# Kernel tuning notes

Measured on AMD Instinct MI355X. Metric: run time of the kernel, lower is better.

Reference implementation:

```python
import jax, jax.numpy as jnp
import numpy as np

D_MODEL = 1024
NUM_HEADS = 16
DEPTH = D_MODEL // NUM_HEADS


def setup_inputs() -> dict:
    key = jax.random.key(0)
    ks = jax.random.split(key, 5)
    s = 1.0 / np.sqrt(D_MODEL)
    return {
        "x": jax.random.normal(ks[0], (4, 2048, D_MODEL), dtype=jnp.float32),
        "wq": jax.random.normal(ks[1], (D_MODEL, D_MODEL), dtype=jnp.float32) * s,
        "bq": jnp.zeros((D_MODEL,), dtype=jnp.float32),
        "wk": jax.random.normal(ks[2], (D_MODEL, D_MODEL), dtype=jnp.float32) * s,
        "bk": jnp.zeros((D_MODEL,), dtype=jnp.float32),
        "wv": jax.random.normal(ks[3], (D_MODEL, D_MODEL), dtype=jnp.float32) * s,
        "bv": jnp.zeros((D_MODEL,), dtype=jnp.float32),
        "wo": jax.random.normal(ks[4], (D_MODEL, D_MODEL), dtype=jnp.float32) * s,
        "bo": jnp.zeros((D_MODEL,), dtype=jnp.float32),
    }


def reference(x, wq, bq, wk, bk, wv, bv, wo, bo):
    B, S, _ = x.shape
    def split_heads(t):  # [B,S,D] -> [B,H,S,depth]
        return t.reshape(B, S, NUM_HEADS, DEPTH).transpose(0, 2, 1, 3)
    q = split_heads(x @ wq + bq)
    k = split_heads(x @ wk + bk)
    v = split_heads(x @ wv + bv)
    scale = 1.0 / jnp.sqrt(jnp.float32(DEPTH))
    logits = jnp.einsum("bhqd,bhkd->bhqk", q, k) * scale
    attn = jax.nn.softmax(logits, axis=-1)  # dropout is identity at inference
    out = jnp.einsum("bhqk,bhkd->bhqd", attn, v)
    out = out.transpose(0, 2, 1, 3).reshape(B, S, D_MODEL)
    return out @ wo + bo
```

## Files before the change

### kernel.cpp

```cpp
#include <hip/hip_runtime.h>
#include <hip/hip_bf16.h>
#include <cstdint>
#include <cstddef>

typedef __attribute__((ext_vector_type(8))) short s8v;
typedef __attribute__((ext_vector_type(4))) float f4v;

#define MFMA_BF16(a, b, c) __builtin_amdgcn_mfma_f32_16x16x32_bf16((a), (b), (c), 0, 0, 0)

__device__ __forceinline__ short f2bf(float f) {
    unsigned u = __builtin_bit_cast(unsigned, f);
    u += 0x7FFFu + ((u >> 16) & 1u);
    return (short)(u >> 16);
}

__device__ __forceinline__ unsigned cvt_pk_bf16(float a, float b) {
    unsigned r;
    asm("v_cvt_pk_bf16_f32 %0, %1, %2" : "=v"(r) : "v"(a), "v"(b));
    return r;
}

#define GLDS16(gsrc, ldst)                                                                   \
    __builtin_amdgcn_global_load_lds(                                                        \
        (const __attribute__((address_space(1))) unsigned int*)(gsrc),                       \
        (__attribute__((address_space(3))) unsigned int*)(ldst), 16, 0, 0)

__global__ void convert_x(const float4* __restrict__ in, short4* __restrict__ out, int n4) {
    int i = blockIdx.x * blockDim.x + threadIdx.x;
    int stride = gridDim.x * blockDim.x;
    for (; i < n4; i += stride) {
        float4 v = in[i];
        short4 o;
        o.x = f2bf(v.x); o.y = f2bf(v.y); o.z = f2bf(v.z); o.w = f2bf(v.w);
        out[i] = o;
    }
}

__global__ void transpose_w(const float* __restrict__ a0, const float* __restrict__ a1,
                            const float* __restrict__ a2, const float* __restrict__ a3,
                            short* __restrict__ outb) {
    const float* src = (blockIdx.z == 0) ? a0 : (blockIdx.z == 1) ? a1 : (blockIdx.z == 2) ? a2 : a3;
    short* dst = outb + (size_t)blockIdx.z * 1048576;
    __shared__ float t[32][33];
    const int n0 = blockIdx.x * 32, k0 = blockIdx.y * 32;
    const int tid = threadIdx.x;
    const int rr = tid >> 3, c4 = (tid & 7) * 4;
    float4 v = *(const float4*)(src + (size_t)(k0 + rr) * 1024 + n0 + c4);
    t[rr][c4 + 0] = v.x; t[rr][c4 + 1] = v.y; t[rr][c4 + 2] = v.z; t[rr][c4 + 3] = v.w;
    __syncthreads();
    short4 o;
    o.x = f2bf(t[c4 + 0][rr]); o.y = f2bf(t[c4 + 1][rr]);
    o.z = f2bf(t[c4 + 2][rr]); o.w = f2bf(t[c4 + 3][rr]);
    *(short4*)(dst + (size_t)(n0 + rr) * 1024 + k0 + c4) = o;
}

template <typename OUT_T, int MODE>
__global__ __launch_bounds__(256, 2) void gemm_bt(const short* __restrict__ A,
                                                  const short* __restrict__ B,
                                                  const float* __restrict__ bias,
                                                  OUT_T* __restrict__ C,
                                                  int M, int N, int K, float alpha) {
    __shared__ short As[128 * 64];
    __shared__ short Bs[128 * 64];
    const int tid = threadIdx.x;
    const int lane = tid & 63;
    const int w = tid >> 6;
    const int wr = w >> 1, wc = w & 1;
    const int m0 = blockIdx.y * 128, n0 = blockIdx.x * 128;
    const int KB = K * 2;

    f4v acc[4][4] = {};

    for (int kt = 0; kt < K; kt += 64) {
#pragma unroll
        for (int i = 0; i < 4; i++) {
            int o = tid * 16 + i * 4096;
            int r = o >> 7;
            int cs = (o & 127) ^ ((r & 7) << 4);
            GLDS16((const char*)A + (size_t)(m0 + r) * KB + kt * 2 + cs,
                   (char*)As + (w * 1024 + i * 4096));
            GLDS16((const char*)B + (size_t)(n0 + r) * KB + kt * 2 + cs,
                   (char*)Bs + (w * 1024 + i * 4096));
        }
        __syncthreads();
#pragma unroll
        for (int kk = 0; kk < 2; kk++) {
            s8v af[4], bf[4];
#pragma unroll
            for (int mi = 0; mi < 4; mi++) {
                int r = wr * 64 + mi * 16 + (lane & 15);
                int cb = (((lane >> 4) * 16) + kk * 64) ^ ((r & 7) << 4);
                af[mi] = *(const s8v*)((const char*)As + r * 128 + cb);
            }
#pragma unroll
            for (int ni = 0; ni < 4; ni++) {
                int r = wc * 64 + ni * 16 + (lane & 15);
                int cb = (((lane >> 4) * 16) + kk * 64) ^ ((r & 7) << 4);
                bf[ni] = *(const s8v*)((const char*)Bs + r * 128 + cb);
            }
#pragma unroll
            for (int mi = 0; mi < 4; mi++)
#pragma unroll
                for (int ni = 0; ni < 4; ni++)
                    acc[mi][ni] = MFMA_BF16(af[mi], bf[ni], acc[mi][ni]);
        }
        __syncthreads();
    }

#pragma unroll
    for (int mi = 0; mi < 4; mi++) {
#pragma unroll
        for (int ni = 0; ni < 4; ni++) {
            int row = m0 + wr * 64 + mi * 16 + ((lane >> 4) << 2);
            int col = n0 + wc * 64 + ni * 16 + (lane & 15);
#pragma unroll
            for (int j = 0; j < 4; j++) {
                float v = acc[mi][ni][j];
                if constexpr (MODE == 0) {
                    v = (v + bias[col]) * alpha;
                    size_t idx = (size_t)(row + j) * N + col;
                    if constexpr (sizeof(OUT_T) == 2) C[idx] = (OUT_T)f2bf(v);
                    else C[idx] = v;
                } else {
                    v = (v + bias[row + j]) * alpha;
                    size_t idx = (size_t)(col >> 11) * (2048 * 1024) + (size_t)(row + j) * 2048 + (col & 2047);
                    C[idx] = (OUT_T)f2bf(v);
                }
            }
        }
    }
}

__global__ __launch_bounds__(256, 3) void attn_fwd(const short* __restrict__ Qb,
                                                   const short* __restrict__ Kb,
                                                   const short* __restrict__ Vtb,
                                                   short* __restrict__ AOb) {
    __shared__ short Ks[2][64 * 64];
    __shared__ short Vs[2][64 * 64];
    __shared__ short Ps[4][32 * 64];

    const int tid = threadIdx.x, lane = tid & 63, w = tid >> 6;
    const int lo = lane & 15, hi = lane >> 4;
    const int qt = blockIdx.x;
    const int bh = blockIdx.y;
    const int b = bh >> 4, h = bh & 15;
    const int q0 = qt * 128 + w * 32;

    s8v qf[2][2];
#pragma unroll
    for (int fr = 0; fr < 2; fr++)
#pragma unroll
        for (int kk = 0; kk < 2; kk++) {
            int row = b * 2048 + q0 + fr * 16 + lo;
            qf[fr][kk] = *(const s8v*)(Qb + (size_t)row * 1024 + h * 64 + hi * 8 + kk * 32);
        }

    f4v oaccT[2][4] = {};
    float m_[2] = {-1e30f, -1e30f};
    float l_[2] = {0.f, 0.f};

    auto STAGE = [&](int s0, int bi) {
#pragma unroll
        for (int i = 0; i < 2; i++) {
            int o = tid * 16 + i * 4096;
            int r = o >> 7;
            int cs = (o & 127) ^ ((r & 7) << 4);
            GLDS16((const char*)Kb + (size_t)(b * 2048 + s0 + r) * 2048 + h * 128 + cs,
                   (char*)Ks[bi] + w * 1024 + i * 4096);
            GLDS16((const char*)Vtb + (size_t)(b * 1024 + h * 64 + r) * 4096 + (size_t)s0 * 2 + cs,
                   (char*)Vs[bi] + w * 1024 + i * 4096);
        }
    };

    STAGE(0, 0);
    __syncthreads();

    int cur = 0;
    for (int t = 0; t < 32; t++) {
        if (t < 31) STAGE((t + 1) * 64, cur ^ 1);

        f4v sf[2][4] = {};
#pragma unroll
        for (int kk = 0; kk < 2; kk++) {
            s8v kf[4];
#pragma unroll
            for (int fc = 0; fc < 4; fc++) {
                int r = fc * 16 + lo;
                int cb = (hi * 16 + kk * 64) ^ ((r & 7) << 4);
                kf[fc] = *(const s8v*)((const char*)Ks[cur] + r * 128 + cb);
            }
#pragma unroll
            for (int fr = 0; fr < 2; fr++)
#pragma unroll
                for (int fc = 0; fc < 4; fc++)
                    sf[fr][fc] = MFMA_BF16(kf[fc], qf[fr][kk], sf[fr][fc]);
        }

#pragma unroll
        for (int fr = 0; fr < 2; fr++) {
            float t0 = fmaxf(fmaxf(sf[fr][0][0], sf[fr][0][1]), fmaxf(sf[fr][0][2], sf[fr][0][3]));
            float t1 = fmaxf(fmaxf(sf[fr][1][0], sf[fr][1][1]), fmaxf(sf[fr][1][2], sf[fr][1][3]));
            float t2 = fmaxf(fmaxf(sf[fr][2][0], sf[fr][2][1]), fmaxf(sf[fr][2][2], sf[fr][2][3]));
            float t3 = fmaxf(fmaxf(sf[fr][3][0], sf[fr][3][1]), fmaxf(sf[fr][3][2], sf[fr][3][3]));
            float tm = fmaxf(fmaxf(t0, t1), fmaxf(t2, t3));
            tm = fmaxf(tm, __shfl_xor(tm, 16, 64));
            tm = fmaxf(tm, __shfl_xor(tm, 32, 64));
            float mn = fmaxf(m_[fr], tm);
            float fac = __builtin_amdgcn_exp2f(m_[fr] - mn);
            m_[fr] = mn;
            float rs = 0.f;
            int q = fr * 16 + lo;
#pragma unroll
            for (int fc = 0; fc < 4; fc++) {
                float p0 = __builtin_amdgcn_exp2f(sf[fr][fc][0] - mn);
                float p1 = __builtin_amdgcn_exp2f(sf[fr][fc][1] - mn);
                float p2 = __builtin_amdgcn_exp2f(sf[fr][fc][2] - mn);
                float p3 = __builtin_amdgcn_exp2f(sf[fr][fc][3] - mn);
                rs += (p0 + p1) + (p2 + p3);
                unsigned pk01 = cvt_pk_bf16(p0, p1);
                unsigned pk23 = cvt_pk_bf16(p2, p3);
                int byte = (q * 128 + fc * 32 + hi * 8) ^ ((q & 7) << 4);
                *(unsigned long long*)((char*)Ps[w] + byte) =
                    ((unsigned long long)pk23 << 32) | pk01;
            }
            rs += __shfl_xor(rs, 16, 64);
            rs += __shfl_xor(rs, 32, 64);
            l_[fr] = l_[fr] * fac + rs;
#pragma unroll
            for (int dv = 0; dv < 4; dv++)
#pragma unroll
                for (int j = 0; j < 4; j++) oaccT[fr][dv][j] *= fac;
        }

#pragma unroll
        for (int kk = 0; kk < 2; kk++) {
            s8v vf[4], pf[2];
#pragma unroll
            for (int fr = 0; fr < 2; fr++) {
                int q = fr * 16 + lo;
                int cb = (kk * 64 + hi * 16) ^ ((q & 7) << 4);
                pf[fr] = *(const s8v*)((const char*)Ps[w] + q * 128 + cb);
            }
#pragma unroll
            for (int dv = 0; dv < 4; dv++) {
                int r = dv * 16 + lo;
                int cb = (kk * 64 + hi * 16) ^ ((r & 7) << 4);
                vf[dv] = *(const s8v*)((const char*)Vs[cur] + r * 128 + cb);
            }
#pragma unroll
            for (int fr = 0; fr < 2; fr++)
#pragma unroll
                for (int dv = 0; dv < 4; dv++)
                    oaccT[fr][dv] = MFMA_BF16(vf[dv], pf[fr], oaccT[fr][dv]);
        }
        __syncthreads();
        cur ^= 1;
    }

#pragma unroll
    for (int fr = 0; fr < 2; fr++) {
        float rl = 1.0f / l_[fr];
        size_t qrow = (size_t)(b * 2048 + q0 + fr * 16 + lo);
#pragma unroll
        for (int dv = 0; dv < 4; dv++) {
            short4 o;
            o.x = f2bf(oaccT[fr][dv][0] * rl);
            o.y = f2bf(oaccT[fr][dv][1] * rl);
            o.z = f2bf(oaccT[fr][dv][2] * rl);
            o.w = f2bf(oaccT[fr][dv][3] * rl);
            *(short4*)(AOb + qrow * 1024 + h * 64 + dv * 16 + hi * 4) = o;
        }
    }
}

extern "C" void kernel_launch(void* const* d_in, const int* in_sizes, int n_in,
                              void* d_out, int out_size, void* d_ws, size_t ws_size,
                              hipStream_t stream) {
    const float* x  = (const float*)d_in[0];
    const float* wq = (const float*)d_in[1];
    const float* bq = (const float*)d_in[2];
    const float* wk = (const float*)d_in[3];
    const float* bk = (const float*)d_in[4];
    const float* wv = (const float*)d_in[5];
    const float* bv = (const float*)d_in[6];
    const float* wo = (const float*)d_in[7];
    const float* bo = (const float*)d_in[8];
    float* out = (float*)d_out;

    char* ws = (char*)d_ws;
    const size_t MB16 = 16777216;
    short* xb  = (short*)(ws);
    short* qb  = (short*)(ws + 1 * MB16);
    short* kb  = (short*)(ws + 2 * MB16);
    short* vtb = (short*)(ws + 3 * MB16);
    short* wT  = (short*)(ws + 4 * MB16);
    short* aob = xb;

    const float qscale = 0.125f * 1.4426950408889634f;

    convert_x<<<dim3(1024), dim3(256), 0, stream>>>((const float4*)x, (short4*)xb, 8388608 / 4);
    transpose_w<<<dim3(32, 32, 4), dim3(256), 0, stream>>>(wq, wk, wv, wo, wT);

    gemm_bt<short, 0><<<dim3(8, 64), dim3(256), 0, stream>>>(xb, wT, bq, qb, 8192, 1024, 1024, qscale);
    gemm_bt<short, 0><<<dim3(8, 64), dim3(256), 0, stream>>>(xb, wT + 1048576, bk, kb, 8192, 1024, 1024, 1.0f);
    gemm_bt<short, 1><<<dim3(64, 8), dim3(256), 0, stream>>>(wT + 2 * 1048576, xb, bv, vtb, 1024, 8192, 1024, 1.0f);

    attn_fwd<<<dim3(16, 64), dim3(256), 0, stream>>>(qb, kb, vtb, aob);

    gemm_bt<float, 0><<<dim3(8, 64), dim3(256), 0, stream>>>(aob, wT + 3 * 1048576, bo, out, 8192, 1024, 1024, 1.0f);
}
```

Measured before the change: 235.4 us.

## Rewrite attention inner loop with 32x32 MFMA and register-resident P

Switches the attention kernel from 16x16x32 to 32x32x16 bf16 MFMA tiles, keeping the P matrix in registers via v_permlane32_swap instead of a round trip through LDS. It adds a lazy rescale that only updates the running max when it grows by more than a threshold, raises launch occupancy to 4 blocks, and adds setprio around MFMA blocks. This aims to cut LDS traffic and per-row softmax shuffles, at the cost of more registers per thread, which may make the higher occupancy target hard to reach.

```diff
diff --git a/kernel.cpp b/kernel.cpp
--- a/kernel.cpp
+++ b/kernel.cpp
@@ -5,8 +5,11 @@
 
 typedef __attribute__((ext_vector_type(8))) short s8v;
 typedef __attribute__((ext_vector_type(4))) float f4v;
+typedef __attribute__((ext_vector_type(16))) float f16v;
+typedef __attribute__((ext_vector_type(4))) unsigned u4v;
 
 #define MFMA_BF16(a, b, c) __builtin_amdgcn_mfma_f32_16x16x32_bf16((a), (b), (c), 0, 0, 0)
+#define MFMA32(a, b, c) __builtin_amdgcn_mfma_f32_32x32x16_bf16((a), (b), (c), 0, 0, 0)
 
 __device__ __forceinline__ short f2bf(float f) {
     unsigned u = __builtin_bit_cast(unsigned, f);
@@ -131,33 +134,27 @@
     }
 }
 
-__global__ __launch_bounds__(256, 3) void attn_fwd(const short* __restrict__ Qb,
+__global__ __launch_bounds__(256, 4) void attn_fwd(const short* __restrict__ Qb,
                                                    const short* __restrict__ Kb,
                                                    const short* __restrict__ Vtb,
                                                    short* __restrict__ AOb) {
     __shared__ short Ks[2][64 * 64];
     __shared__ short Vs[2][64 * 64];
-    __shared__ short Ps[4][32 * 64];
 
     const int tid = threadIdx.x, lane = tid & 63, w = tid >> 6;
-    const int lo = lane & 15, hi = lane >> 4;
+    const int l5 = lane & 31, H = lane >> 5;
     const int qt = blockIdx.x;
     const int bh = blockIdx.y;
     const int b = bh >> 4, h = bh & 15;
     const int q0 = qt * 128 + w * 32;
 
-    s8v qf[2][2];
-#pragma unroll
-    for (int fr = 0; fr < 2; fr++)
-#pragma unroll
-        for (int kk = 0; kk < 2; kk++) {
-            int row = b * 2048 + q0 + fr * 16 + lo;
-            qf[fr][kk] = *(const s8v*)(Qb + (size_t)row * 1024 + h * 64 + hi * 8 + kk * 32);
-        }
-
-    f4v oaccT[2][4] = {};
-    float m_[2] = {-1e30f, -1e30f};
-    float l_[2] = {0.f, 0.f};
+    s8v qf[4];
+#pragma unroll
+    for (int st = 0; st < 4; st++)
+        qf[st] = *(const s8v*)(Qb + (size_t)(b * 2048 + q0 + l5) * 1024 + h * 64 + st * 16 + H * 8);
+
+    f16v oacc[2] = {};
+    float m_ = -1e30f, l_ = 0.f;
 
     auto STAGE = [&](int s0, int bi) {
 #pragma unroll
@@ -179,98 +176,90 @@
     for (int t = 0; t < 32; t++) {
         if (t < 31) STAGE((t + 1) * 64, cur ^ 1);
 
-        f4v sf[2][4] = {};
-#pragma unroll
-        for (int kk = 0; kk < 2; kk++) {
-            s8v kf[4];
-#pragma unroll
-            for (int fc = 0; fc < 4; fc++) {
-                int r = fc * 16 + lo;
-                int cb = (hi * 16 + kk * 64) ^ ((r & 7) << 4);
-                kf[fc] = *(const s8v*)((const char*)Ks[cur] + r * 128 + cb);
-            }
-#pragma unroll
-            for (int fr = 0; fr < 2; fr++)
-#pragma unroll
-                for (int fc = 0; fc < 4; fc++)
-                    sf[fr][fc] = MFMA_BF16(kf[fc], qf[fr][kk], sf[fr][fc]);
-        }
-
-#pragma unroll
-        for (int fr = 0; fr < 2; fr++) {
-            float t0 = fmaxf(fmaxf(sf[fr][0][0], sf[fr][0][1]), fmaxf(sf[fr][0][2], sf[fr][0][3]));
-            float t1 = fmaxf(fmaxf(sf[fr][1][0], sf[fr][1][1]), fmaxf(sf[fr][1][2], sf[fr][1][3]));
-            float t2 = fmaxf(fmaxf(sf[fr][2][0], sf[fr][2][1]), fmaxf(sf[fr][2][2], sf[fr][2][3]));
-            float t3 = fmaxf(fmaxf(sf[fr][3][0], sf[fr][3][1]), fmaxf(sf[fr][3][2], sf[fr][3][3]));
-            float tm = fmaxf(fmaxf(t0, t1), fmaxf(t2, t3));
-            tm = fmaxf(tm, __shfl_xor(tm, 16, 64));
-            tm = fmaxf(tm, __shfl_xor(tm, 32, 64));
-            float mn = fmaxf(m_[fr], tm);
-            float fac = __builtin_amdgcn_exp2f(m_[fr] - mn);
-            m_[fr] = mn;
-            float rs = 0.f;
-            int q = fr * 16 + lo;
-#pragma unroll
-            for (int fc = 0; fc < 4; fc++) {
-                float p0 = __builtin_amdgcn_exp2f(sf[fr][fc][0] - mn);
-                float p1 = __builtin_amdgcn_exp2f(sf[fr][fc][1] - mn);
-                float p2 = __builtin_amdgcn_exp2f(sf[fr][fc][2] - mn);
-                float p3 = __builtin_amdgcn_exp2f(sf[fr][fc][3] - mn);
-                rs += (p0 + p1) + (p2 + p3);
-                unsigned pk01 = cvt_pk_bf16(p0, p1);
-                unsigned pk23 = cvt_pk_bf16(p2, p3);
-                int byte = (q * 128 + fc * 32 + hi * 8) ^ ((q & 7) << 4);
-                *(unsigned long long*)((char*)Ps[w] + byte) =
-                    ((unsigned long long)pk23 << 32) | pk01;
-            }
-            rs += __shfl_xor(rs, 16, 64);
-            rs += __shfl_xor(rs, 32, 64);
-            l_[fr] = l_[fr] * fac + rs;
-#pragma unroll
-            for (int dv = 0; dv < 4; dv++)
-#pragma unroll
-                for (int j = 0; j < 4; j++) oaccT[fr][dv][j] *= fac;
-        }
-
-#pragma unroll
-        for (int kk = 0; kk < 2; kk++) {
-            s8v vf[4], pf[2];
-#pragma unroll
-            for (int fr = 0; fr < 2; fr++) {
-                int q = fr * 16 + lo;
-                int cb = (kk * 64 + hi * 16) ^ ((q & 7) << 4);
-                pf[fr] = *(const s8v*)((const char*)Ps[w] + q * 128 + cb);
-            }
-#pragma unroll
-            for (int dv = 0; dv < 4; dv++) {
-                int r = dv * 16 + lo;
-                int cb = (kk * 64 + hi * 16) ^ ((r & 7) << 4);
-                vf[dv] = *(const s8v*)((const char*)Vs[cur] + r * 128 + cb);
-            }
-#pragma unroll
-            for (int fr = 0; fr < 2; fr++)
-#pragma unroll
-                for (int dv = 0; dv < 4; dv++)
-                    oaccT[fr][dv] = MFMA_BF16(vf[dv], pf[fr], oaccT[fr][dv]);
+        f16v sf[2] = {};
+        __builtin_amdgcn_s_setprio(1);
+#pragma unroll
+        for (int kt = 0; kt < 2; kt++) {
+            int r = kt * 32 + l5;
+            int swz = (r & 7) << 4;
+#pragma unroll
+            for (int st = 0; st < 4; st++) {
+                s8v kf = *(const s8v*)((const char*)Ks[cur] + r * 128 + ((st * 32 + H * 16) ^ swz));
+                sf[kt] = MFMA32(kf, qf[st], sf[kt]);
+            }
+        }
+        __builtin_amdgcn_s_setprio(0);
+
+        float mx[16];
+#pragma unroll
+        for (int i = 0; i < 16; i++) mx[i] = fmaxf(sf[0][i], sf[1][i]);
+#pragma unroll
+        for (int stp = 8; stp >= 1; stp >>= 1)
+#pragma unroll
+            for (int i = 0; i < stp; i++) mx[i] = fmaxf(mx[i], mx[i + stp]);
+        float tm = fmaxf(mx[0], __shfl_xor(mx[0], 32, 64));
+
+        if (!__all(tm - m_ <= 8.0f)) {
+            float mn = fmaxf(m_, tm);
+            float fac = __builtin_amdgcn_exp2f(m_ - mn);
+            m_ = mn;
+            l_ *= fac;
+#pragma unroll
+            for (int dt = 0; dt < 2; dt++)
+#pragma unroll
+                for (int i = 0; i < 16; i++) oacc[dt][i] *= fac;
+        }
+
+        float rs0 = 0.f, rs1 = 0.f;
+#pragma unroll
+        for (int kt = 0; kt < 2; kt++)
+#pragma unroll
+            for (int i = 0; i < 16; i++) {
+                float p = __builtin_amdgcn_exp2f(sf[kt][i] - m_);
+                sf[kt][i] = p;
+                if (i & 1) rs1 += p; else rs0 += p;
+            }
+        float rs = rs0 + rs1;
+        rs += __shfl_xor(rs, 32, 64);
+        l_ += rs;
+
+#pragma unroll
+        for (int s = 0; s < 4; s++) {
+            const int kt = s >> 1, base = (s & 1) * 8;
+            unsigned dA0 = cvt_pk_bf16(sf[kt][base + 0], sf[kt][base + 1]);
+            unsigned dA1 = cvt_pk_bf16(sf[kt][base + 2], sf[kt][base + 3]);
+            unsigned dB0 = cvt_pk_bf16(sf[kt][base + 4], sf[kt][base + 5]);
+            unsigned dB1 = cvt_pk_bf16(sf[kt][base + 6], sf[kt][base + 7]);
+            asm("v_permlane32_swap_b32 %0, %1" : "+v"(dA0), "+v"(dB0));
+            asm("v_permlane32_swap_b32 %0, %1" : "+v"(dA1), "+v"(dB1));
+            u4v fw = {dA0, dA1, dB0, dB1};
+            s8v pfrag = __builtin_bit_cast(s8v, fw);
+            __builtin_amdgcn_s_setprio(1);
+#pragma unroll
+            for (int dt = 0; dt < 2; dt++) {
+                int r = dt * 32 + l5;
+                s8v vf = *(const s8v*)((const char*)Vs[cur] + r * 128 + ((s * 32 + H * 16) ^ ((r & 7) << 4)));
+                oacc[dt] = MFMA32(vf, pfrag, oacc[dt]);
+            }
+            __builtin_amdgcn_s_setprio(0);
         }
         __syncthreads();
         cur ^= 1;
     }
 
-#pragma unroll
-    for (int fr = 0; fr < 2; fr++) {
-        float rl = 1.0f / l_[fr];
-        size_t qrow = (size_t)(b * 2048 + q0 + fr * 16 + lo);
-#pragma unroll
-        for (int dv = 0; dv < 4; dv++) {
+    float rl = 1.0f / l_;
+    size_t orow = (size_t)(b * 2048 + q0 + l5) * 1024 + h * 64;
+#pragma unroll
+    for (int dt = 0; dt < 2; dt++)
+#pragma unroll
+        for (int g = 0; g < 4; g++) {
             short4 o;
-            o.x = f2bf(oaccT[fr][dv][0] * rl);
-            o.y = f2bf(oaccT[fr][dv][1] * rl);
-            o.z = f2bf(oaccT[fr][dv][2] * rl);
-            o.w = f2bf(oaccT[fr][dv][3] * rl);
-            *(short4*)(AOb + qrow * 1024 + h * 64 + dv * 16 + hi * 4) = o;
-        }
-    }
+            o.x = f2bf(oacc[dt][4 * g + 0] * rl);
+            o.y = f2bf(oacc[dt][4 * g + 1] * rl);
+            o.z = f2bf(oacc[dt][4 * g + 2] * rl);
+            o.w = f2bf(oacc[dt][4 * g + 3] * rl);
+            *(short4*)(AOb + orow + dt * 32 + g * 8 + H * 4) = o;
+        }
 }
 
 extern "C" void kernel_launch(void* const* d_in, const int* in_sizes, int n_in,
```

New measurement: 211.8 us. -10.0%, faster.
